# Performance work log

Measured on AMD Instinct MI355X. Metric: run time of the kernel, lower is better.

## Reference

```python
import jax, jax.numpy as jnp
import numpy as np

SIG = [1, 1, 1, 1, -1]  # Cl(4,1)
GA_DIM = 1 << len(SIG)  # 32
IN_F, OUT_F = 128, 128
EPS = 1e-6


def _cayley(sig):
    """Dense Cayley tensor C[a,b,k]: e_a * e_b = C[a,b,a^b] * e_{a^b}.
    Only dim^2 of the dim^3 entries are nonzero (one k per (a,b))."""
    n = len(sig)
    dim = 1 << n
    C = np.zeros((dim, dim, dim), dtype=np.float32)
    for a in range(dim):
        for b in range(dim):
            # reordering sign from moving b's generators past a's
            s = 0
            aa = a >> 1
            while aa:
                s += bin(aa & b).count('1')
                aa >>= 1
            sign = -1.0 if (s & 1) else 1.0
            # metric contribution from repeated generators
            common = a & b
            for i in range(n):
                if common & (1 << i):
                    sign *= sig[i]
            C[a, b, a ^ b] = sign
    return C

_C = jnp.asarray(_cayley(SIG))  # [32,32,32]


def setup_inputs() -> dict:
    key = jax.random.key(0)
    kx, kw = jax.random.split(key)
    x = jax.random.normal(kx, (4096, IN_F, GA_DIM), dtype=jnp.float32)
    std = (2.0 / (IN_F * GA_DIM)) ** 0.5
    w = jax.random.normal(kw, (OUT_F, IN_F, GA_DIM), dtype=jnp.float32) * std
    return {"x": x, "weight": w}


def reference(x, weight):
    # Fold Cayley table into the weight once: Wc[o,f,i,k] = sum_j W[o,f,j] C[i,j,k]
    Wc = jnp.einsum('ofj,ijk->ofik', weight, _C)
    # Geometric linear layer: y[b,o,k] = sum_{f,i} x[b,f,i] Wc[o,f,i,k]
    y = jnp.einsum('bfi,ofik->bok', x, Wc)
    # Manifold normalization: project each output multivector to unit norm
    inv = jax.lax.rsqrt(jnp.sum(y * y, axis=-1, keepdims=True) + EPS)
    return y * inv
```

## Files before the change

### kernel.cpp

```cpp
#include <hip/hip_runtime.h>
#include <stdint.h>

typedef unsigned short ushort_t;
typedef __attribute__((ext_vector_type(8)))  __bf16 bf16x8;
typedef __attribute__((ext_vector_type(16))) float  f32x16;


__device__ __forceinline__ unsigned int f2bf(float f) {
    unsigned int u = __float_as_uint(f);
    return (u + 0x7FFFu + ((u >> 16) & 1u)) >> 16;
}

__device__ __forceinline__ float cayley_sign(int a, int b) {
    int s = 0;
    int aa = a >> 1;
    while (aa) { s += __popc(aa & b); aa >>= 1; }
    float sign = (s & 1) ? -1.0f : 1.0f;
    if (a & b & 16) sign = -sign;
    return sign;
}

__device__ __forceinline__ void async16(const ushort_t* g, const ushort_t* l) {
    const __attribute__((address_space(1))) unsigned int* gp =
        (const __attribute__((address_space(1))) unsigned int*)(uintptr_t)g;
    __attribute__((address_space(3))) unsigned int* lp =
        (__attribute__((address_space(3))) unsigned int*)(unsigned int)(uintptr_t)l;
    __builtin_amdgcn_global_load_lds(gp, lp, 16, 0, 0);
}

__global__ __launch_bounds__(256) void prepAB(const float* __restrict__ x,
                                              const float* __restrict__ w,
                                              ushort_t* __restrict__ A_sw,
                                              ushort_t* __restrict__ B_sw) {
    const int k_blk = blockIdx.x;
    const int p_blk = blockIdx.y >> 1;
    const int sub   = blockIdx.y & 1;
    const int t = threadIdx.x;
    const int r  = sub * 64 + (t >> 2);
    const int kq = t & 3;

    if (blockIdx.z == 0) {
        const float* src = x + (size_t)(p_blk * 128 + r) * 4096 + (size_t)k_blk * 32 + kq * 8;
        float4 a = ((const float4*)src)[0];
        float4 b = ((const float4*)src)[1];
        uint4 pk;
        pk.x = f2bf(a.x) | (f2bf(a.y) << 16);
        pk.y = f2bf(a.z) | (f2bf(a.w) << 16);
        pk.z = f2bf(b.x) | (f2bf(b.y) << 16);
        pk.w = f2bf(b.z) | (f2bf(b.w) << 16);
        ushort_t* chunk = A_sw + ((size_t)p_blk * 128 + k_blk) * 4096;
        *(uint4*)(chunk + kq * 1024 + r * 8) = pk;
    } else {
        const int n = p_blk * 128 + r;
        const int o = n >> 5;
        const int kc = n & 31;
        const float* wrow = w + (size_t)o * 4096 + (size_t)k_blk * 32;
        unsigned int pk[4];
#pragma unroll
        for (int pr = 0; pr < 4; ++pr) {
            const int i0 = kq * 8 + pr * 2, i1 = i0 + 1;
            const int j0 = i0 ^ kc, j1 = i1 ^ kc;
            float v0 = wrow[j0] * cayley_sign(i0, j0);
            float v1 = wrow[j1] * cayley_sign(i1, j1);
            pk[pr] = f2bf(v0) | (f2bf(v1) << 16);
        }
        uint4 u = {pk[0], pk[1], pk[2], pk[3]};
        ushort_t* chunk = B_sw + ((size_t)p_blk * 128 + k_blk) * 4096;
        *(uint4*)(chunk + kq * 1024 + r * 8) = u;
    }
}

__global__ __launch_bounds__(256) void gemm_norm(const ushort_t* __restrict__ A_sw,
                                                 const ushort_t* __restrict__ B_sw,
                                                 float* __restrict__ out) {
    __shared__ ushort_t As[2][4096];
    __shared__ ushort_t Bs[2][4096];

    const int n_blk = blockIdx.x;
    const int m_blk = blockIdx.y;
    const int t = threadIdx.x;
    const int wave = t >> 6;
    const int lane = t & 63;
    const int half = lane >> 5;
    const int l32  = lane & 31;
    const int wr = wave >> 1;
    const int wc = wave & 1;

    f32x16 acc[2][2];
#pragma unroll
    for (int a = 0; a < 2; ++a)
#pragma unroll
        for (int b = 0; b < 2; ++b)
#pragma unroll
            for (int i = 0; i < 16; ++i) acc[a][b][i] = 0.0f;

    const ushort_t* aPanel = A_sw + (size_t)m_blk * 128 * 4096;
    const ushort_t* bPanel = B_sw + (size_t)n_blk * 128 * 4096;

    async16(aPanel + t * 8,        As[0] + wave * 512);
    async16(aPanel + 2048 + t * 8, As[0] + 2048 + wave * 512);
    async16(bPanel + t * 8,        Bs[0] + wave * 512);
    async16(bPanel + 2048 + t * 8, Bs[0] + 2048 + wave * 512);

    for (int kb = 0; kb < 128; ++kb) {
        const int cur = kb & 1;
        __syncthreads();

        if (kb + 1 < 128) {
            const ushort_t* gA = aPanel + (size_t)(kb + 1) * 4096;
            const ushort_t* gB = bPanel + (size_t)(kb + 1) * 4096;
            const int nxt = cur ^ 1;
            async16(gA + t * 8,        As[nxt] + wave * 512);
            async16(gA + 2048 + t * 8, As[nxt] + 2048 + wave * 512);
            async16(gB + t * 8,        Bs[nxt] + wave * 512);
            async16(gB + 2048 + t * 8, Bs[nxt] + 2048 + wave * 512);
        }

        bf16x8 aF[2][2], bF[2][2];
#pragma unroll
        for (int tm = 0; tm < 2; ++tm)
#pragma unroll
            for (int kh = 0; kh < 2; ++kh)
                aF[tm][kh] = *(const bf16x8*)&As[cur][(kh * 2 + half) * 1024 + (wr * 64 + tm * 32 + l32) * 8];
#pragma unroll
        for (int tn = 0; tn < 2; ++tn)
#pragma unroll
            for (int kh = 0; kh < 2; ++kh)
                bF[tn][kh] = *(const bf16x8*)&Bs[cur][(kh * 2 + half) * 1024 + (wc * 64 + tn * 32 + l32) * 8];

#pragma unroll
        for (int tm = 0; tm < 2; ++tm)
#pragma unroll
            for (int tn = 0; tn < 2; ++tn) {
                acc[tm][tn] = __builtin_amdgcn_mfma_f32_32x32x16_bf16(aF[tm][0], bF[tn][0], acc[tm][tn], 0, 0, 0);
                acc[tm][tn] = __builtin_amdgcn_mfma_f32_32x32x16_bf16(aF[tm][1], bF[tn][1], acc[tm][tn], 0, 0, 0);
            }
    }

    const int row0 = m_blk * 128 + wr * 64;
    const int col0 = n_blk * 128 + wc * 64;
#pragma unroll
    for (int tm = 0; tm < 2; ++tm) {
#pragma unroll
        for (int tn = 0; tn < 2; ++tn) {
            const int cbase = col0 + tn * 32 + l32;
#pragma unroll
            for (int reg = 0; reg < 16; ++reg) {
                float v = acc[tm][tn][reg];
                float p = v * v;
                p += __shfl_xor(p, 1);
                p += __shfl_xor(p, 2);
                p += __shfl_xor(p, 4);
                p += __shfl_xor(p, 8);
                p += __shfl_xor(p, 16);
                const float inv = rsqrtf(p + 1e-6f);
                const int row = row0 + tm * 32 + (reg & 3) + 8 * (reg >> 2) + 4 * half;
                out[(size_t)row * 4096 + cbase] = v * inv;
            }
        }
    }
}


extern "C" void kernel_launch(void* const* d_in, const int* in_sizes, int n_in,
                              void* d_out, int out_size, void* d_ws, size_t ws_size,
                              hipStream_t stream) {
    const float* x = (const float*)d_in[0];
    const float* w = (const float*)d_in[1];
    float* out = (float*)d_out;

    ushort_t* A_sw = (ushort_t*)d_ws;
    ushort_t* B_sw = A_sw + (size_t)4096 * 4096;

    prepAB<<<dim3(128, 64, 2), 256, 0, stream>>>(x, w, A_sw, B_sw);
    gemm_norm<<<dim3(32, 32), 256, 0, stream>>>(A_sw, B_sw, out);
}
```

Measured before the change: 279.5 us.

## Fuse x fp32-to-bf16 conversion into GEMM A-tile loading, shrink prep kernel

The A operand is no longer pre-converted into a bf16 workspace. Each GEMM block now loads fp32 x rows directly, converts them to bf16 in registers and stores them into LDS, overlapping the global loads with the MFMA work. The prep kernel now only builds the Cayley-folded B and uses fewer blocks, each looping 8 times. This removes a full write and re-read of the 32MB bf16 A buffer, but each GEMM block re-reads fp32 x (twice the bytes of bf16), and x is re-read by the 32 column blocks.

```diff
diff --git a/kernel.cpp b/kernel.cpp
--- a/kernel.cpp
+++ b/kernel.cpp
@@ -28,31 +28,19 @@
     __builtin_amdgcn_global_load_lds(gp, lp, 16, 0, 0);
 }
 
-__global__ __launch_bounds__(256) void prepAB(const float* __restrict__ x,
-                                              const float* __restrict__ w,
-                                              ushort_t* __restrict__ A_sw,
-                                              ushort_t* __restrict__ B_sw) {
-    const int k_blk = blockIdx.x;
-    const int p_blk = blockIdx.y >> 1;
-    const int sub   = blockIdx.y & 1;
+__global__ __launch_bounds__(256) void prepB(const float* __restrict__ w,
+                                             ushort_t* __restrict__ B_sw) {
     const int t = threadIdx.x;
-    const int r  = sub * 64 + (t >> 2);
     const int kq = t & 3;
-
-    if (blockIdx.z == 0) {
-        const float* src = x + (size_t)(p_blk * 128 + r) * 4096 + (size_t)k_blk * 32 + kq * 8;
-        float4 a = ((const float4*)src)[0];
-        float4 b = ((const float4*)src)[1];
-        uint4 pk;
-        pk.x = f2bf(a.x) | (f2bf(a.y) << 16);
-        pk.y = f2bf(a.z) | (f2bf(a.w) << 16);
-        pk.z = f2bf(b.x) | (f2bf(b.y) << 16);
-        pk.w = f2bf(b.z) | (f2bf(b.w) << 16);
-        ushort_t* chunk = A_sw + ((size_t)p_blk * 128 + k_blk) * 4096;
-        *(uint4*)(chunk + kq * 1024 + r * 8) = pk;
-    } else {
-        const int n = p_blk * 128 + r;
-        const int o = n >> 5;
+#pragma unroll
+    for (int i = 0; i < 8; ++i) {
+        const int vb = blockIdx.x + i * 1024;
+        const int k_blk = vb & 127;
+        const int y     = vb >> 7;
+        const int p_blk = y >> 1;
+        const int r     = (y & 1) * 64 + (t >> 2);
+        const int n  = p_blk * 128 + r;
+        const int o  = n >> 5;
         const int kc = n & 31;
         const float* wrow = w + (size_t)o * 4096 + (size_t)k_blk * 32;
         unsigned int pk[4];
@@ -70,7 +58,7 @@
     }
 }
 
-__global__ __launch_bounds__(256) void gemm_norm(const ushort_t* __restrict__ A_sw,
+__global__ __launch_bounds__(256) void gemm_norm(const float* __restrict__ x,
                                                  const ushort_t* __restrict__ B_sw,
                                                  float* __restrict__ out) {
     __shared__ ushort_t As[2][4096];
@@ -86,6 +74,9 @@
     const int wr = wave >> 1;
     const int wc = wave & 1;
 
+    const int ar  = t >> 1;
+    const int kh2 = t & 1;
+
     f32x16 acc[2][2];
 #pragma unroll
     for (int a = 0; a < 2; ++a)
@@ -94,26 +85,39 @@
 #pragma unroll
             for (int i = 0; i < 16; ++i) acc[a][b][i] = 0.0f;
 
-    const ushort_t* aPanel = A_sw + (size_t)m_blk * 128 * 4096;
+    const float* xRow = x + (size_t)(m_blk * 128 + ar) * 4096 + kh2 * 16;
     const ushort_t* bPanel = B_sw + (size_t)n_blk * 128 * 4096;
 
-    async16(aPanel + t * 8,        As[0] + wave * 512);
-    async16(aPanel + 2048 + t * 8, As[0] + 2048 + wave * 512);
     async16(bPanel + t * 8,        Bs[0] + wave * 512);
     async16(bPanel + 2048 + t * 8, Bs[0] + 2048 + wave * 512);
+    {
+        const float4* src = (const float4*)(xRow);
+        float4 f0 = src[0], f1 = src[1], f2 = src[2], f3 = src[3];
+        uint4 p0, p1;
+        p0.x = f2bf(f0.x) | (f2bf(f0.y) << 16);
+        p0.y = f2bf(f0.z) | (f2bf(f0.w) << 16);
+        p0.z = f2bf(f1.x) | (f2bf(f1.y) << 16);
+        p0.w = f2bf(f1.z) | (f2bf(f1.w) << 16);
+        p1.x = f2bf(f2.x) | (f2bf(f2.y) << 16);
+        p1.y = f2bf(f2.z) | (f2bf(f2.w) << 16);
+        p1.z = f2bf(f3.x) | (f2bf(f3.y) << 16);
+        p1.w = f2bf(f3.z) | (f2bf(f3.w) << 16);
+        *(uint4*)&As[0][(2 * kh2) * 1024 + ar * 8]     = p0;
+        *(uint4*)&As[0][(2 * kh2 + 1) * 1024 + ar * 8] = p1;
+    }
 
     for (int kb = 0; kb < 128; ++kb) {
         const int cur = kb & 1;
+        const int nxt = cur ^ 1;
         __syncthreads();
 
+        float4 f0, f1, f2, f3;
         if (kb + 1 < 128) {
-            const ushort_t* gA = aPanel + (size_t)(kb + 1) * 4096;
             const ushort_t* gB = bPanel + (size_t)(kb + 1) * 4096;
-            const int nxt = cur ^ 1;
-            async16(gA + t * 8,        As[nxt] + wave * 512);
-            async16(gA + 2048 + t * 8, As[nxt] + 2048 + wave * 512);
             async16(gB + t * 8,        Bs[nxt] + wave * 512);
             async16(gB + 2048 + t * 8, Bs[nxt] + 2048 + wave * 512);
+            const float4* src = (const float4*)(xRow + (size_t)(kb + 1) * 32);
+            f0 = src[0]; f1 = src[1]; f2 = src[2]; f3 = src[3];
         }
 
         bf16x8 aF[2][2], bF[2][2];
@@ -135,6 +139,20 @@
                 acc[tm][tn] = __builtin_amdgcn_mfma_f32_32x32x16_bf16(aF[tm][0], bF[tn][0], acc[tm][tn], 0, 0, 0);
                 acc[tm][tn] = __builtin_amdgcn_mfma_f32_32x32x16_bf16(aF[tm][1], bF[tn][1], acc[tm][tn], 0, 0, 0);
             }
+
+        if (kb + 1 < 128) {
+            uint4 p0, p1;
+            p0.x = f2bf(f0.x) | (f2bf(f0.y) << 16);
+            p0.y = f2bf(f0.z) | (f2bf(f0.w) << 16);
+            p0.z = f2bf(f1.x) | (f2bf(f1.y) << 16);
+            p0.w = f2bf(f1.z) | (f2bf(f1.w) << 16);
+            p1.x = f2bf(f2.x) | (f2bf(f2.y) << 16);
+            p1.y = f2bf(f2.z) | (f2bf(f2.w) << 16);
+            p1.z = f2bf(f3.x) | (f2bf(f3.y) << 16);
+            p1.w = f2bf(f3.z) | (f2bf(f3.w) << 16);
+            *(uint4*)&As[nxt][(2 * kh2) * 1024 + ar * 8]     = p0;
+            *(uint4*)&As[nxt][(2 * kh2 + 1) * 1024 + ar * 8] = p1;
+        }
     }
 
     const int row0 = m_blk * 128 + wr * 64;
@@ -169,9 +187,8 @@
     const float* w = (const float*)d_in[1];
     float* out = (float*)d_out;
 
-    ushort_t* A_sw = (ushort_t*)d_ws;
-    ushort_t* B_sw = A_sw + (size_t)4096 * 4096;
+    ushort_t* B_sw = (ushort_t*)d_ws;
 
-    prepAB<<<dim3(128, 64, 2), 256, 0, stream>>>(x, w, A_sw, B_sw);
-    gemm_norm<<<dim3(32, 32), 256, 0, stream>>>(A_sw, B_sw, out);
+    prepB<<<dim3(1024), 256, 0, stream>>>(w, B_sw);
+    gemm_norm<<<dim3(32, 32), 256, 0, stream>>>(x, B_sw, out);
 }
```

Measured after the change: 426.7 us. 52.7% more time.

## Load A fragments directly from global, double K-step per stage, swizzle block order

Applied to the files above, without the earlier changes.

The GEMM stops staging A through LDS. Each wave reads its A fragments straight from global memory, while only B is double-buffered in shared memory, with 64 K per iteration instead of 32. This halves the number of barriers and frees LDS. Block indices are remapped into 4x8 supertiles so concurrently running blocks share A/B panels in L2. The risk is that global A loads now sit on the MFMA critical path without prefetch, and each wave re-reads the same A rows as its sibling wave.

```diff
diff --git a/kernel.cpp b/kernel.cpp
--- a/kernel.cpp
+++ b/kernel.cpp
@@ -73,11 +73,13 @@
 __global__ __launch_bounds__(256) void gemm_norm(const ushort_t* __restrict__ A_sw,
                                                  const ushort_t* __restrict__ B_sw,
                                                  float* __restrict__ out) {
-    __shared__ ushort_t As[2][4096];
-    __shared__ ushort_t Bs[2][4096];
+    __shared__ ushort_t Bs[2][8192];
 
-    const int n_blk = blockIdx.x;
-    const int m_blk = blockIdx.y;
+    const int bid = blockIdx.x;
+    const int sup = bid >> 5;
+    const int m_blk = (sup >> 2) * 4 + ((bid >> 3) & 3);
+    const int n_blk = (sup & 3) * 8 + (bid & 7);
+
     const int t = threadIdx.x;
     const int wave = t >> 6;
     const int lane = t & 63;
@@ -97,44 +99,47 @@
     const ushort_t* aPanel = A_sw + (size_t)m_blk * 128 * 4096;
     const ushort_t* bPanel = B_sw + (size_t)n_blk * 128 * 4096;
 
-    async16(aPanel + t * 8,        As[0] + wave * 512);
-    async16(aPanel + 2048 + t * 8, As[0] + 2048 + wave * 512);
-    async16(bPanel + t * 8,        Bs[0] + wave * 512);
-    async16(bPanel + 2048 + t * 8, Bs[0] + 2048 + wave * 512);
+    const int rA0 = wr * 64 + 0  + l32;
+    const int rA1 = wr * 64 + 32 + l32;
+    const int cB  = wc * 64 + l32;
 
-    for (int kb = 0; kb < 128; ++kb) {
+#pragma unroll
+    for (int i = 0; i < 4; ++i)
+        async16(bPanel + i * 2048 + t * 8, Bs[0] + i * 2048 + t * 8);
+
+    for (int kb = 0; kb < 64; ++kb) {
         const int cur = kb & 1;
         __syncthreads();
 
-        if (kb + 1 < 128) {
-            const ushort_t* gA = aPanel + (size_t)(kb + 1) * 4096;
-            const ushort_t* gB = bPanel + (size_t)(kb + 1) * 4096;
-            const int nxt = cur ^ 1;
-            async16(gA + t * 8,        As[nxt] + wave * 512);
-            async16(gA + 2048 + t * 8, As[nxt] + 2048 + wave * 512);
-            async16(gB + t * 8,        Bs[nxt] + wave * 512);
-            async16(gB + 2048 + t * 8, Bs[nxt] + 2048 + wave * 512);
+        if (kb + 1 < 64) {
+            const ushort_t* gB = bPanel + (size_t)(kb + 1) * 8192;
+#pragma unroll
+            for (int i = 0; i < 4; ++i)
+                async16(gB + i * 2048 + t * 8, Bs[cur ^ 1] + i * 2048 + t * 8);
         }
 
-        bf16x8 aF[2][2], bF[2][2];
+        const ushort_t* gA = aPanel + (size_t)kb * 8192;
+        bf16x8 aF[2][4], bF[2][4];
 #pragma unroll
-        for (int tm = 0; tm < 2; ++tm)
+        for (int ks = 0; ks < 4; ++ks) {
+            const int el = (ks >> 1) * 4096 + ((ks & 1) * 2 + half) * 1024;
+            aF[0][ks] = *(const bf16x8*)(gA + el + rA0 * 8);
+            aF[1][ks] = *(const bf16x8*)(gA + el + rA1 * 8);
+        }
 #pragma unroll
-            for (int kh = 0; kh < 2; ++kh)
-                aF[tm][kh] = *(const bf16x8*)&As[cur][(kh * 2 + half) * 1024 + (wr * 64 + tm * 32 + l32) * 8];
-#pragma unroll
-        for (int tn = 0; tn < 2; ++tn)
-#pragma unroll
-            for (int kh = 0; kh < 2; ++kh)
-                bF[tn][kh] = *(const bf16x8*)&Bs[cur][(kh * 2 + half) * 1024 + (wc * 64 + tn * 32 + l32) * 8];
+        for (int ks = 0; ks < 4; ++ks) {
+            const int el = (ks >> 1) * 4096 + ((ks & 1) * 2 + half) * 1024;
+            bF[0][ks] = *(const bf16x8*)&Bs[cur][el + cB * 8];
+            bF[1][ks] = *(const bf16x8*)&Bs[cur][el + (cB + 32) * 8];
+        }
 
 #pragma unroll
-        for (int tm = 0; tm < 2; ++tm)
-#pragma unroll
-            for (int tn = 0; tn < 2; ++tn) {
-                acc[tm][tn] = __builtin_amdgcn_mfma_f32_32x32x16_bf16(aF[tm][0], bF[tn][0], acc[tm][tn], 0, 0, 0);
-                acc[tm][tn] = __builtin_amdgcn_mfma_f32_32x32x16_bf16(aF[tm][1], bF[tn][1], acc[tm][tn], 0, 0, 0);
-            }
+        for (int ks = 0; ks < 4; ++ks) {
+            acc[0][0] = __builtin_amdgcn_mfma_f32_32x32x16_bf16(aF[0][ks], bF[0][ks], acc[0][0], 0, 0, 0);
+            acc[0][1] = __builtin_amdgcn_mfma_f32_32x32x16_bf16(aF[0][ks], bF[1][ks], acc[0][1], 0, 0, 0);
+            acc[1][0] = __builtin_amdgcn_mfma_f32_32x32x16_bf16(aF[1][ks], bF[0][ks], acc[1][0], 0, 0, 0);
+            acc[1][1] = __builtin_amdgcn_mfma_f32_32x32x16_bf16(aF[1][ks], bF[1][ks], acc[1][1], 0, 0, 0);
+        }
     }
 
     const int row0 = m_blk * 128 + wr * 64;
@@ -173,5 +178,5 @@
     ushort_t* B_sw = A_sw + (size_t)4096 * 4096;
 
     prepAB<<<dim3(128, 64, 2), 256, 0, stream>>>(x, w, A_sw, B_sw);
-    gemm_norm<<<dim3(32, 32), 256, 0, stream>>>(A_sw, B_sw, out);
+    gemm_norm<<<dim3(1024), 256, 0, stream>>>(A_sw, B_sw, out);
 }
```

Measured after the change: 352.3 us. 1.26x slower.
